# Kernel tuning notes

Measured on AMD Instinct MI355X. Metric: run time of the kernel, lower is better.

The kernel has to match this reference:

```python
import jax, jax.numpy as jnp
import numpy as np

DIM = 512
HEADS = 8
HEAD_DIM = DIM // HEADS


def setup_inputs() -> dict:
    key = jax.random.key(0)
    ks = jax.random.split(key, 8)
    B, T, C, H, W = 2, 8, DIM, 16, 16
    s = lambda fan: 1.0 / np.sqrt(fan)
    return {
        "features_seq": jax.random.normal(ks[0], (B, T, C, H, W), jnp.float32),
        # weights stored as [in, out] (math identical to torch Linear y = x @ W.T)
        "qkv_w": jax.random.normal(ks[1], (C, 3 * C), jnp.float32) * s(C),
        "qkv_b": jnp.zeros((3 * C,), jnp.float32),
        "proj_w": jax.random.normal(ks[2], (C, C), jnp.float32) * s(C),
        "proj_b": jnp.zeros((C,), jnp.float32),
        "ln1_g": jnp.ones((C,), jnp.float32),
        "ln1_b": jnp.zeros((C,), jnp.float32),
        "w1": jax.random.normal(ks[3], (C, 4 * C), jnp.float32) * s(C),
        "b1": jnp.zeros((4 * C,), jnp.float32),
        "w2": jax.random.normal(ks[4], (4 * C, C), jnp.float32) * s(4 * C),
        "b2": jnp.zeros((C,), jnp.float32),
        "ln2_g": jnp.ones((C,), jnp.float32),
        "ln2_b": jnp.zeros((C,), jnp.float32),
    }


def _layernorm(x, g, b, eps=1e-5):
    mu = jnp.mean(x, axis=-1, keepdims=True)
    var = jnp.var(x, axis=-1, keepdims=True)
    return (x - mu) * jax.lax.rsqrt(var + eps) * g + b


def _mhsa(x, qkv_w, qkv_b, proj_w, proj_b):
    B, N, C = x.shape
    qkv = (x @ qkv_w + qkv_b).reshape(B, N, 3, HEADS, HEAD_DIM)
    qkv = jnp.transpose(qkv, (2, 0, 3, 1, 4))  # [3, B, h, N, d]
    q, k, v = qkv[0], qkv[1], qkv[2]
    scale = HEAD_DIM ** -0.5
    attn = jnp.einsum("bhqd,bhkd->bhqk", q, k) * scale
    attn = jax.nn.softmax(attn, axis=-1)
    o = jnp.einsum("bhqk,bhkd->bhqd", attn, v)
    o = jnp.transpose(o, (0, 2, 1, 3)).reshape(B, N, C)
    return o @ proj_w + proj_b


def reference(features_seq, qkv_w, qkv_b, proj_w, proj_b, ln1_g, ln1_b,
              w1, b1, w2, b2, ln2_g, ln2_b):
    B, T, C, H, W = features_seq.shape
    L = H * W
    # [B,T,C,H,W] -> [B, T*L, C]
    x = features_seq.reshape(B, T, C, L).transpose(0, 1, 3, 2).reshape(B, T * L, C)
    x = x + _mhsa(_layernorm(x, ln1_g, ln1_b), qkv_w, qkv_b, proj_w, proj_b)
    h = _layernorm(x, ln2_g, ln2_b)
    h = jax.nn.gelu(h @ w1 + b1, approximate=False) @ w2 + b2
    x = x + h
    # back to [B, T, C, H, W]
    out = x.reshape(B, T, L, C).transpose(0, 1, 3, 2).reshape(B, T, C, H, W)
    return out
```

## Files before the change

kernel.cpp:

```cpp
#include <hip/hip_runtime.h>
#include <stdint.h>
#include <math.h>

typedef __attribute__((ext_vector_type(8))) short short8;
typedef __attribute__((ext_vector_type(4))) float f32x4;

__device__ __forceinline__ ushort f2bf(float f) {
    union { float f; uint32_t i; } v; v.f = f;
    uint32_t r = v.i + 0x7FFFu + ((v.i >> 16) & 1u);
    return (ushort)(r >> 16);
}
__device__ __forceinline__ float bf2f(ushort u) {
    union { uint32_t i; float f; } v; v.i = ((uint32_t)u) << 16; return v.f;
}

__global__ __launch_bounds__(512) void prep_kernel(const float* __restrict__ in,
        const float* __restrict__ g, const float* __restrict__ bta,
        float* __restrict__ x, ushort* __restrict__ xln) {
    int token = blockIdx.x;
    int c = threadIdx.x;
    int b = token >> 11;
    int n = token & 2047;
    int t = n >> 8;
    int l = n & 255;
    size_t iidx = (((size_t)((b * 8 + t) * 512 + c)) << 8) + l;
    float v = in[iidx];
    x[(size_t)token * 512 + c] = v;

    float s = v, s2 = v * v;
    #pragma unroll
    for (int off = 32; off > 0; off >>= 1) {
        s  += __shfl_down(s, off, 64);
        s2 += __shfl_down(s2, off, 64);
    }
    __shared__ float ps[8], ps2[8];
    int wave = threadIdx.x >> 6, lane = threadIdx.x & 63;
    if (lane == 0) { ps[wave] = s; ps2[wave] = s2; }
    __syncthreads();
    float mu = 0.f, m2 = 0.f;
    #pragma unroll
    for (int i = 0; i < 8; i++) { mu += ps[i]; m2 += ps2[i]; }
    mu *= (1.0f / 512.0f); m2 *= (1.0f / 512.0f);
    float rs = rsqrtf(m2 - mu * mu + 1e-5f);
    float y = (v - mu) * rs * g[c] + bta[c];
    xln[(size_t)token * 512 + c] = f2bf(y);
}

__global__ __launch_bounds__(512) void ln2_kernel(const float* __restrict__ xin,
        const float* __restrict__ g, const float* __restrict__ bta,
        ushort* __restrict__ out) {
    int token = blockIdx.x;
    int c = threadIdx.x;
    float v = xin[(size_t)token * 512 + c];
    float s = v, s2 = v * v;
    #pragma unroll
    for (int off = 32; off > 0; off >>= 1) {
        s  += __shfl_down(s, off, 64);
        s2 += __shfl_down(s2, off, 64);
    }
    __shared__ float ps[8], ps2[8];
    int wave = threadIdx.x >> 6, lane = threadIdx.x & 63;
    if (lane == 0) { ps[wave] = s; ps2[wave] = s2; }
    __syncthreads();
    float mu = 0.f, m2 = 0.f;
    #pragma unroll
    for (int i = 0; i < 8; i++) { mu += ps[i]; m2 += ps2[i]; }
    mu *= (1.0f / 512.0f); m2 *= (1.0f / 512.0f);
    float rs = rsqrtf(m2 - mu * mu + 1e-5f);
    float y = (v - mu) * rs * g[c] + bta[c];
    out[(size_t)token * 512 + c] = f2bf(y);
}

#define EPI_BF16   0
#define EPI_F32RES 1
#define EPI_GELU   2

template<int EPI>
__global__ __launch_bounds__(256) void gemm_kernel(
        const ushort* __restrict__ A, const float* __restrict__ Bw,
        const float* __restrict__ bias, const float* __restrict__ resid,
        float* __restrict__ outF, ushort* __restrict__ outB,
        int M, int N, int K) {
    __shared__ __align__(16) ushort As[64][40];
    __shared__ __align__(16) ushort Bs[64][40];
    int tid = threadIdx.x;
    int wave = tid >> 6, lane = tid & 63;
    int l16 = lane & 15, quad = lane >> 4;
    int m0 = blockIdx.y * 64, n0 = blockIdx.x * 64;
    int am = tid >> 2, ak = (tid & 3) * 8;
    int bn = tid & 63, bk = (tid >> 6) * 8;
    f32x4 acc[4] = {};
    for (int k0 = 0; k0 < K; k0 += 32) {
        *(short8*)&As[am][ak] = *(const short8*)(A + (size_t)(m0 + am) * K + k0 + ak);
        short8 bv;
        #pragma unroll
        for (int i = 0; i < 8; i++)
            bv[i] = (short)f2bf(Bw[(size_t)(k0 + bk + i) * N + n0 + bn]);
        *(short8*)&Bs[bn][bk] = bv;
        __syncthreads();
        short8 af = *(short8*)&As[wave * 16 + l16][quad * 8];
        #pragma unroll
        for (int s = 0; s < 4; s++) {
            short8 bf = *(short8*)&Bs[s * 16 + l16][quad * 8];
            acc[s] = __builtin_amdgcn_mfma_f32_16x16x32_bf16(af, bf, acc[s], 0, 0, 0);
        }
        __syncthreads();
    }
    int row_base = m0 + wave * 16 + quad * 4;
    #pragma unroll
    for (int s = 0; s < 4; s++) {
        int col = n0 + s * 16 + l16;
        float bvf = bias[col];
        #pragma unroll
        for (int r = 0; r < 4; r++) {
            int row = row_base + r;
            float v = acc[s][r] + bvf;
            if constexpr (EPI == EPI_F32RES) {
                outF[(size_t)row * N + col] = v + resid[(size_t)row * N + col];
            } else if constexpr (EPI == EPI_GELU) {
                float gg = 0.5f * v * (1.0f + erff(v * 0.70710678118654752f));
                outB[(size_t)row * N + col] = f2bf(gg);
            } else {
                outB[(size_t)row * N + col] = f2bf(v);
            }
        }
    }
}

__global__ __launch_bounds__(512) void flash_kernel(const ushort* __restrict__ qkv,
        ushort* __restrict__ o) {
    __shared__ __align__(16) char smem[55424];
    auto Ks  = (ushort (*)[64][72])smem;
    auto Vt  = (ushort (*)[4640])(smem + 18432);
    auto Pt  = (ushort (*)[16][72])(smem + 36992);
    auto cbuf = (float (*)[24][64])smem;

    int tid = threadIdx.x;
    int wave = tid >> 6, lane = tid & 63;
    int kh = wave >> 2;
    int wq = wave & 3;
    int l16 = lane & 15, quad = lane >> 4;
    int bidx = blockIdx.x;
    int qt = bidx & 31;
    int h = (bidx >> 5) & 7;
    int b = bidx >> 8;
    int q0 = qt * 64;
    const size_t base = (size_t)b * 2048 * 1536;

    int htid = tid & 255;
    int srow = htid >> 2;
    int sg   = htid & 3;
    int sdb  = sg * 16;
    const ushort* kgbase = qkv + base + 512  + h * 64 + sdb;
    const ushort* vgbase = qkv + base + 1024 + h * 64 + sdb;
    int vldsoff = sdb * 72 + sg * 8 + srow;

    short8 aq[2];
    {
        int qrow = q0 + wq * 16 + l16;
        const ushort* qp = qkv + base + (size_t)qrow * 1536 + h * 64;
        aq[0] = *(const short8*)(qp + quad * 8);
        aq[1] = *(const short8*)(qp + 32 + quad * 8);
    }
    f32x4 accO[4] = {};
    float mrow[4] = {-INFINITY, -INFINITY, -INFINITY, -INFINITY};
    float lrow[4] = {0.f, 0.f, 0.f, 0.f};

    {
        int kb = kh * 1024;
        const ushort* kp = kgbase + (size_t)(kb + srow) * 1536;
        short8 k0 = *(const short8*)kp;
        short8 k1 = *(const short8*)(kp + 8);
        const ushort* vp = vgbase + (size_t)(kb + srow) * 1536;
        short8 v0 = *(const short8*)vp;
        short8 v1 = *(const short8*)(vp + 8);
        *(short8*)&Ks[kh][srow][sdb]     = k0;
        *(short8*)&Ks[kh][srow][sdb + 8] = k1;
        #pragma unroll
        for (int i = 0; i < 8; i++) Vt[kh][vldsoff + i * 72] = (ushort)v0[i];
        #pragma unroll
        for (int i = 0; i < 8; i++) Vt[kh][vldsoff + (8 + i) * 72] = (ushort)v1[i];
    }
    __syncthreads();

    for (int it = 0; it < 16; ++it) {
        short8 nk0, nk1, nv0, nv1;
        bool pre = (it < 15);
        if (pre) {
            int kb = kh * 1024 + (it + 1) * 64;
            const ushort* kp = kgbase + (size_t)(kb + srow) * 1536;
            nk0 = *(const short8*)kp;
            nk1 = *(const short8*)(kp + 8);
            const ushort* vp = vgbase + (size_t)(kb + srow) * 1536;
            nv0 = *(const short8*)vp;
            nv1 = *(const short8*)(vp + 8);
        }
        f32x4 sacc[4] = {};
        __builtin_amdgcn_s_setprio(1);
        #pragma unroll
        for (int c = 0; c < 2; c++) {
            #pragma unroll
            for (int s = 0; s < 4; s++) {
                short8 kf = *(short8*)&Ks[kh][s * 16 + l16][c * 32 + quad * 8];
                sacc[s] = __builtin_amdgcn_mfma_f32_16x16x32_bf16(aq[c], kf, sacc[s], 0, 0, 0);
            }
        }
        __builtin_amdgcn_s_setprio(0);
        float p[4][4];
        #pragma unroll
        for (int r = 0; r < 4; r++) {
            float tm = fmaxf(fmaxf(sacc[0][r], sacc[1][r]), fmaxf(sacc[2][r], sacc[3][r]));
            #pragma unroll
            for (int off = 1; off < 16; off <<= 1)
                tm = fmaxf(tm, __shfl_xor(tm, off, 16));
            float mn = fmaxf(mrow[r], tm * 0.125f);
            float al = __expf(mrow[r] - mn);
            float rsum = 0.f;
            #pragma unroll
            for (int s = 0; s < 4; s++) {
                float pv = __expf(sacc[s][r] * 0.125f - mn);
                p[s][r] = pv;
                rsum += pv;
            }
            #pragma unroll
            for (int off = 1; off < 16; off <<= 1)
                rsum += __shfl_xor(rsum, off, 16);
            lrow[r] = lrow[r] * al + rsum;
            mrow[r] = mn;
            #pragma unroll
            for (int s = 0; s < 4; s++) accO[s][r] *= al;
        }
        #pragma unroll
        for (int s = 0; s < 4; s++)
            #pragma unroll
            for (int r = 0; r < 4; r++)
                Pt[wave][quad * 4 + r][s * 16 + l16] = f2bf(p[s][r]);
        __builtin_amdgcn_s_setprio(1);
        #pragma unroll
        for (int ks = 0; ks < 2; ks++) {
            short8 ap = *(short8*)&Pt[wave][l16][ks * 32 + quad * 8];
            #pragma unroll
            for (int s = 0; s < 4; s++) {
                short8 vf = *(short8*)&Vt[kh][(s * 16 + l16) * 72 + s * 8 + ks * 32 + quad * 8];
                accO[s] = __builtin_amdgcn_mfma_f32_16x16x32_bf16(ap, vf, accO[s], 0, 0, 0);
            }
        }
        __builtin_amdgcn_s_setprio(0);
        __syncthreads();
        if (pre) {
            *(short8*)&Ks[kh][srow][sdb]     = nk0;
            *(short8*)&Ks[kh][srow][sdb + 8] = nk1;
            #pragma unroll
            for (int i = 0; i < 8; i++) Vt[kh][vldsoff + i * 72] = (ushort)nv0[i];
            #pragma unroll
            for (int i = 0; i < 8; i++) Vt[kh][vldsoff + (8 + i) * 72] = (ushort)nv1[i];
        }
        __syncthreads();
    }
    if (kh == 1) {
        #pragma unroll
        for (int r = 0; r < 4; r++) {
            cbuf[wq][r][lane]     = mrow[r];
            cbuf[wq][4 + r][lane] = lrow[r];
        }
        #pragma unroll
        for (int s = 0; s < 4; s++)
            #pragma unroll
            for (int r = 0; r < 4; r++)
                cbuf[wq][8 + s * 4 + r][lane] = accO[s][r];
    }
    __syncthreads();
    if (kh == 0) {
        #pragma unroll
        for (int r = 0; r < 4; r++) {
            float m1 = cbuf[wq][r][lane];
            float l1 = cbuf[wq][4 + r][lane];
            float mn = fmaxf(mrow[r], m1);
            float a0 = __expf(mrow[r] - mn);
            float a1 = __expf(m1 - mn);
            float rl = 1.0f / (lrow[r] * a0 + l1 * a1);
            int qrow = q0 + wq * 16 + quad * 4 + r;
            #pragma unroll
            for (int s = 0; s < 4; s++) {
                float ov = (accO[s][r] * a0 + cbuf[wq][8 + s * 4 + r][lane] * a1) * rl;
                o[((size_t)(b * 2048 + qrow)) * 512 + h * 64 + s * 16 + l16] = f2bf(ov);
            }
        }
    }
}

__global__ __launch_bounds__(256) void tout_kernel(const float* __restrict__ x3,
        float* __restrict__ out) {
    __shared__ float tile[32][33];
    int bt = blockIdx.z;
    int l0 = blockIdx.y * 32;
    int c0 = blockIdx.x * 32;
    int tx = threadIdx.x, ty = threadIdx.y;
    #pragma unroll
    for (int i = 0; i < 4; i++) {
        int l = ty + i * 8;
        tile[l][tx] = x3[((size_t)bt * 256 + l0 + l) * 512 + c0 + tx];
    }
    __syncthreads();
    #pragma unroll
    for (int i = 0; i < 4; i++) {
        int cc = ty + i * 8;
        out[((size_t)bt * 512 + c0 + cc) * 256 + l0 + tx] = tile[tx][cc];
    }
}

extern "C" void kernel_launch(void* const* d_in, const int* in_sizes, int n_in,
                              void* d_out, int out_size, void* d_ws, size_t ws_size,
                              hipStream_t stream) {
    const float* in_feat = (const float*)d_in[0];
    const float* qkv_w  = (const float*)d_in[1];
    const float* qkv_b  = (const float*)d_in[2];
    const float* proj_w = (const float*)d_in[3];
    const float* proj_b = (const float*)d_in[4];
    const float* ln1_g  = (const float*)d_in[5];
    const float* ln1_b  = (const float*)d_in[6];
    const float* w1     = (const float*)d_in[7];
    const float* b1     = (const float*)d_in[8];
    const float* w2     = (const float*)d_in[9];
    const float* b2     = (const float*)d_in[10];
    const float* ln2_g  = (const float*)d_in[11];
    const float* ln2_b  = (const float*)d_in[12];

    char* ws = (char*)d_ws;
    float*  x    = (float*) (ws);
    float*  x2   = (float*) (ws + 8388608);
    ushort* xln  = (ushort*)(ws + 16777216);
    ushort* h2   = (ushort*)(ws + 20971520);
    ushort* ao   = (ushort*)(ws + 25165824);
    ushort* qkv  = (ushort*)(ws + 29360128);
    ushort* gbuf = (ushort*)(ws + 41943040);

    prep_kernel<<<4096, 512, 0, stream>>>(in_feat, ln1_g, ln1_b, x, xln);
    gemm_kernel<EPI_BF16><<<dim3(24, 64), 256, 0, stream>>>(
        xln, qkv_w, qkv_b, nullptr, nullptr, qkv, 4096, 1536, 512);
    flash_kernel<<<512, 512, 0, stream>>>(qkv, ao);
    gemm_kernel<EPI_F32RES><<<dim3(8, 64), 256, 0, stream>>>(
        ao, proj_w, proj_b, x, x2, nullptr, 4096, 512, 512);
    ln2_kernel<<<4096, 512, 0, stream>>>(x2, ln2_g, ln2_b, h2);
    gemm_kernel<EPI_GELU><<<dim3(32, 64), 256, 0, stream>>>(
        h2, w1, b1, nullptr, nullptr, gbuf, 4096, 2048, 512);
    gemm_kernel<EPI_F32RES><<<dim3(8, 64), 256, 0, stream>>>(
        gbuf, w2, b2, x2, x, nullptr, 4096, 512, 2048);
    tout_kernel<<<dim3(16, 8, 16), dim3(32, 8), 0, stream>>>(x, (float*)d_out);
}
```

Baseline: 275.9 us.

## Pre-transpose weights to bf16 and use larger swizzled GEMM tiles with direct-to-LDS loads

```diff
diff --git a/kernel.cpp b/kernel.cpp
--- a/kernel.cpp
+++ b/kernel.cpp
@@ -12,6 +12,12 @@
 }
 __device__ __forceinline__ float bf2f(ushort u) {
     union { uint32_t i; float f; } v; v.i = ((uint32_t)u) << 16; return v.f;
+}
+
+__device__ __forceinline__ void gload_lds16(const ushort* gp, ushort* lp) {
+    __builtin_amdgcn_global_load_lds(
+        (const __attribute__((address_space(1))) void*)gp,
+        (__attribute__((address_space(3))) void*)lp, 16, 0, 0);
 }
 
 __global__ __launch_bounds__(512) void prep_kernel(const float* __restrict__ in,
@@ -71,57 +77,108 @@
     out[(size_t)token * 512 + c] = f2bf(y);
 }
 
+__global__ __launch_bounds__(256) void wtrans_kernel(
+        const float* __restrict__ wa, ushort* __restrict__ ta,
+        const float* __restrict__ wb, ushort* __restrict__ tb,
+        const float* __restrict__ wc, ushort* __restrict__ tc,
+        const float* __restrict__ wd, ushort* __restrict__ td) {
+    __shared__ float tile[32][33];
+    int bid = blockIdx.x;
+    const float* W; ushort* T; int K, N, tn, tk;
+    if (bid < 768)       { W = wa; T = ta; K = 512;  N = 1536; tn = bid % 48; tk = bid / 48; }
+    else if (bid < 1024) { bid -= 768;  W = wb; T = tb; K = 512;  N = 512;  tn = bid % 16; tk = bid / 16; }
+    else if (bid < 2048) { bid -= 1024; W = wc; T = tc; K = 512;  N = 2048; tn = bid % 64; tk = bid / 64; }
+    else                 { bid -= 2048; W = wd; T = td; K = 2048; N = 512;  tn = bid % 16; tk = bid / 16; }
+    int n0 = tn * 32, k0 = tk * 32;
+    int tx = threadIdx.x & 31, ty = threadIdx.x >> 5;
+    #pragma unroll
+    for (int i = 0; i < 4; i++)
+        tile[ty + i * 8][tx] = W[(size_t)(k0 + ty + i * 8) * N + n0 + tx];
+    __syncthreads();
+    #pragma unroll
+    for (int i = 0; i < 4; i++) {
+        int nn = ty + i * 8;
+        T[(size_t)(n0 + nn) * K + k0 + tx] = f2bf(tile[tx][nn]);
+    }
+}
+
 #define EPI_BF16   0
 #define EPI_F32RES 1
 #define EPI_GELU   2
 
 template<int EPI>
 __global__ __launch_bounds__(256) void gemm_kernel(
-        const ushort* __restrict__ A, const float* __restrict__ Bw,
+        const ushort* __restrict__ A, const ushort* __restrict__ Bt,
         const float* __restrict__ bias, const float* __restrict__ resid,
         float* __restrict__ outF, ushort* __restrict__ outB,
         int M, int N, int K) {
-    __shared__ __align__(16) ushort As[64][40];
-    __shared__ __align__(16) ushort Bs[64][40];
+    __shared__ __align__(16) ushort As[64 * 64];
+    __shared__ __align__(16) ushort Bs[128 * 64];
     int tid = threadIdx.x;
     int wave = tid >> 6, lane = tid & 63;
     int l16 = lane & 15, quad = lane >> 4;
-    int m0 = blockIdx.y * 64, n0 = blockIdx.x * 64;
-    int am = tid >> 2, ak = (tid & 3) * 8;
-    int bn = tid & 63, bk = (tid >> 6) * 8;
-    f32x4 acc[4] = {};
-    for (int k0 = 0; k0 < K; k0 += 32) {
-        *(short8*)&As[am][ak] = *(const short8*)(A + (size_t)(m0 + am) * K + k0 + ak);
-        short8 bv;
-        #pragma unroll
-        for (int i = 0; i < 8; i++)
-            bv[i] = (short)f2bf(Bw[(size_t)(k0 + bk + i) * N + n0 + bn]);
-        *(short8*)&Bs[bn][bk] = bv;
+    int wc = wave;
+    int m0 = blockIdx.y * 64, n0 = blockIdx.x * 128;
+
+    f32x4 acc[4][2] = {};
+    for (int k0 = 0; k0 < K; k0 += 64) {
+        #pragma unroll
+        for (int c = 0; c < 2; c++) {
+            int e = c * 256 + tid;
+            int row = e >> 3, ch = e & 7;
+            int sc = ch ^ (row & 7);
+            gload_lds16(A + (size_t)(m0 + row) * K + k0 + sc * 8,
+                        As + (size_t)(c * 256 + wave * 64) * 8);
+        }
+        #pragma unroll
+        for (int c = 0; c < 4; c++) {
+            int e = c * 256 + tid;
+            int row = e >> 3, ch = e & 7;
+            int sc = ch ^ (row & 7);
+            gload_lds16(Bt + (size_t)(n0 + row) * K + k0 + sc * 8,
+                        Bs + (size_t)(c * 256 + wave * 64) * 8);
+        }
         __syncthreads();
-        short8 af = *(short8*)&As[wave * 16 + l16][quad * 8];
-        #pragma unroll
-        for (int s = 0; s < 4; s++) {
-            short8 bf = *(short8*)&Bs[s * 16 + l16][quad * 8];
-            acc[s] = __builtin_amdgcn_mfma_f32_16x16x32_bf16(af, bf, acc[s], 0, 0, 0);
+        #pragma unroll
+        for (int kk = 0; kk < 2; kk++) {
+            short8 af[4], bf[2];
+            #pragma unroll
+            for (int i = 0; i < 4; i++) {
+                int row = i * 16 + l16;
+                af[i] = *(const short8*)&As[row * 64 + (((kk * 4 + quad) ^ (row & 7)) * 8)];
+            }
+            #pragma unroll
+            for (int j = 0; j < 2; j++) {
+                int row = wc * 32 + j * 16 + l16;
+                bf[j] = *(const short8*)&Bs[row * 64 + (((kk * 4 + quad) ^ (row & 7)) * 8)];
+            }
+            #pragma unroll
+            for (int i = 0; i < 4; i++)
+                #pragma unroll
+                for (int j = 0; j < 2; j++)
+                    acc[i][j] = __builtin_amdgcn_mfma_f32_16x16x32_bf16(af[i], bf[j], acc[i][j], 0, 0, 0);
         }
         __syncthreads();
     }
-    int row_base = m0 + wave * 16 + quad * 4;
-    #pragma unroll
-    for (int s = 0; s < 4; s++) {
-        int col = n0 + s * 16 + l16;
-        float bvf = bias[col];
-        #pragma unroll
-        for (int r = 0; r < 4; r++) {
-            int row = row_base + r;
-            float v = acc[s][r] + bvf;
-            if constexpr (EPI == EPI_F32RES) {
-                outF[(size_t)row * N + col] = v + resid[(size_t)row * N + col];
-            } else if constexpr (EPI == EPI_GELU) {
-                float gg = 0.5f * v * (1.0f + erff(v * 0.70710678118654752f));
-                outB[(size_t)row * N + col] = f2bf(gg);
-            } else {
-                outB[(size_t)row * N + col] = f2bf(v);
+    #pragma unroll
+    for (int i = 0; i < 4; i++) {
+        int row_base = m0 + i * 16 + quad * 4;
+        #pragma unroll
+        for (int j = 0; j < 2; j++) {
+            int col = n0 + wc * 32 + j * 16 + l16;
+            float bvf = bias[col];
+            #pragma unroll
+            for (int r = 0; r < 4; r++) {
+                int row = row_base + r;
+                float v = acc[i][j][r] + bvf;
+                if constexpr (EPI == EPI_F32RES) {
+                    outF[(size_t)row * N + col] = v + resid[(size_t)row * N + col];
+                } else if constexpr (EPI == EPI_GELU) {
+                    float gg = 0.5f * v * (1.0f + erff(v * 0.70710678118654752f));
+                    outB[(size_t)row * N + col] = f2bf(gg);
+                } else {
+                    outB[(size_t)row * N + col] = f2bf(v);
+                }
             }
         }
     }
@@ -335,16 +392,24 @@
     ushort* qkv  = (ushort*)(ws + 29360128);
     ushort* gbuf = (ushort*)(ws + 41943040);
 
+    char* scr = (char*)d_out;
+    ushort* qkvT = (ushort*)(scr);
+    ushort* projT = (ushort*)(scr + 1572864);
+    ushort* w1T  = (ushort*)(scr + 2097152);
+    ushort* w2T  = (ushort*)(scr + 4194304);
+
+    wtrans_kernel<<<3072, 256, 0, stream>>>(qkv_w, qkvT, proj_w, projT,
+                                            w1, w1T, w2, w2T);
     prep_kernel<<<4096, 512, 0, stream>>>(in_feat, ln1_g, ln1_b, x, xln);
-    gemm_kernel<EPI_BF16><<<dim3(24, 64), 256, 0, stream>>>(
-        xln, qkv_w, qkv_b, nullptr, nullptr, qkv, 4096, 1536, 512);
+    gemm_kernel<EPI_BF16><<<dim3(12, 64), 256, 0, stream>>>(
+        xln, qkvT, qkv_b, nullptr, nullptr, qkv, 4096, 1536, 512);
     flash_kernel<<<512, 512, 0, stream>>>(qkv, ao);
-    gemm_kernel<EPI_F32RES><<<dim3(8, 64), 256, 0, stream>>>(
-        ao, proj_w, proj_b, x, x2, nullptr, 4096, 512, 512);
+    gemm_kernel<EPI_F32RES><<<dim3(4, 64), 256, 0, stream>>>(
+        ao, projT, proj_b, x, x2, nullptr, 4096, 512, 512);
     ln2_kernel<<<4096, 512, 0, stream>>>(x2, ln2_g, ln2_b, h2);
-    gemm_kernel<EPI_GELU><<<dim3(32, 64), 256, 0, stream>>>(
-        h2, w1, b1, nullptr, nullptr, gbuf, 4096, 2048, 512);
-    gemm_kernel<EPI_F32RES><<<dim3(8, 64), 256, 0, stream>>>(
-        gbuf, w2, b2, x2, x, nullptr, 4096, 512, 2048);
+    gemm_kernel<EPI_GELU><<<dim3(16, 64), 256, 0, stream>>>(
+        h2, w1T, b1, nullptr, nullptr, gbuf, 4096, 2048, 512);
+    gemm_kernel<EPI_F32RES><<<dim3(4, 64), 256, 0, stream>>>(
+        gbuf, w2T, b2, x2, x, nullptr, 4096, 512, 2048);
     tout_kernel<<<dim3(16, 8, 16), dim3(32, 8), 0, stream>>>(x, (float*)d_out);
 }
```

Result: faster. 254.2 us (-7.8%).
